# Kernel optimization log

Measured on AMD Instinct MI355X. Metric: run time of the kernel, lower is better.

## Reference

```python
import jax, jax.numpy as jnp
import numpy as np
import math

N_HEAD = 16

def setup_inputs() -> dict:
    key = jax.random.key(0)
    ks = jax.random.split(key, 8)
    B, S, P, NX = 4, 1024, 128, 1024
    return {
        "x": jax.random.normal(ks[0], (B, S, NX), jnp.float32),
        "M": jax.random.normal(ks[1], (B, P, NX), jnp.float32),
        "Mmask": jnp.ones((B, P), jnp.float32),
        "attention_mask": jnp.zeros((B, 1, 1, S), jnp.float32),
        "W_attn": jax.random.normal(ks[2], (NX, 3 * NX), jnp.float32) * 0.02,
        "b_attn": jnp.zeros((3 * NX,), jnp.float32),
        "W_mem": jax.random.normal(ks[3], (NX, 2 * NX), jnp.float32) * 0.02,
        "b_mem": jnp.zeros((2 * NX,), jnp.float32),
        "W_proj": jax.random.normal(ks[4], (NX, NX), jnp.float32) * 0.02,
        "b_proj": jnp.zeros((NX,), jnp.float32),
    }

def _split_heads(t, H):
    B, T, NX = t.shape
    return t.reshape(B, T, H, NX // H).transpose(0, 2, 1, 3)  # [B,H,T,dh]

def reference(x, M, Mmask, attention_mask, W_attn, b_attn, W_mem, b_mem, W_proj, b_proj):
    B, S, NX = x.shape
    H = N_HEAD
    dh = NX // H
    P = M.shape[1]

    # fused QKV projection (Conv1D == x @ W + b)
    qkv = x @ W_attn + b_attn
    q, k, v = jnp.split(qkv, 3, axis=2)

    # memory K/V projection, prepended along the key/value sequence axis
    ekv = M @ W_mem + b_mem
    ek, ev = jnp.split(ekv, 2, axis=2)
    key = jnp.concatenate([ek, k], axis=1)   # [B, P+S, NX]
    value = jnp.concatenate([ev, v], axis=1)

    qh = _split_heads(q, H)      # [B,H,S,dh]
    kh = _split_heads(key, H)    # [B,H,P+S,dh]
    vh = _split_heads(value, H)  # [B,H,P+S,dh]

    w = jnp.einsum('bhsd,bhtd->bhst', qh, kh) / math.sqrt(dh)  # [B,H,S,P+S]

    # causal bias over the self part, all-ones over the memory part
    causal = jnp.tril(jnp.ones((S, S), w.dtype))
    b = jnp.concatenate([jnp.ones((S, P), w.dtype), causal], axis=1)[None, None]  # [1,1,S,P+S]
    w = w * b - 10000.0 * (1.0 - b)

    # additive attention mask: memory-mask bias concatenated before token mask
    mem_bias = (1.0 - Mmask)[:, None, None, :] * -10000.0  # [B,1,1,P]
    am = jnp.concatenate([mem_bias, jnp.broadcast_to(attention_mask, (B, 1, 1, S))], axis=3)
    w = w + am

    w = jax.nn.softmax(w, axis=-1)
    a = jnp.einsum('bhst,bhtd->bhsd', w, vh)                  # [B,H,S,dh]
    a = a.transpose(0, 2, 1, 3).reshape(B, S, NX)             # merge heads
    return a @ W_proj + b_proj
```

## Files before the change

kernel.cpp:

```cpp
#include <hip/hip_runtime.h>
#include <hip/hip_bf16.h>


typedef __attribute__((ext_vector_type(8))) short bf16x8;
typedef __attribute__((ext_vector_type(4))) float f32x4;

#define MFMA16(a, b, c) __builtin_amdgcn_mfma_f32_16x16x32_bf16((a), (b), (c), 0, 0, 0)

#define GLOAD_LDS16(g, l)                                                  \
    __builtin_amdgcn_global_load_lds(                                      \
        (const __attribute__((address_space(1))) void*)(const void*)(g),   \
        (__attribute__((address_space(3))) void*)(void*)(l), 16, 0, 0)

static __device__ __forceinline__ unsigned short f2bf(float f) {
    union { float f; unsigned int u; } v; v.f = f;
    unsigned int u = v.u;
    return (unsigned short)((u + 0x7fffu + ((u >> 16) & 1u)) >> 16);
}

__global__ void cvt_all(const float* __restrict__ x, const float* __restrict__ Mem,
                        unsigned short* __restrict__ x_bf, unsigned short* __restrict__ M_bf) {
    int i = blockIdx.x * 256 + threadIdx.x;
    if (i < 1048576) {
        float4 v = ((const float4*)x)[i];
        ushort4 o; o.x = f2bf(v.x); o.y = f2bf(v.y); o.z = f2bf(v.z); o.w = f2bf(v.w);
        ((ushort4*)x_bf)[i] = o;
    } else {
        int j = i - 1048576;
        float4 v = ((const float4*)Mem)[j];
        ushort4 o; o.x = f2bf(v.x); o.y = f2bf(v.y); o.z = f2bf(v.z); o.w = f2bf(v.w);
        ((ushort4*)M_bf)[j] = o;
    }
}

static __device__ __forceinline__ void transpose_body(const float* __restrict__ W,
                                                      unsigned short* __restrict__ Wt,
                                                      int K, int N, int bx, int by,
                                                      float (*tile)[33]) {
    int n0 = bx * 32, k0 = by * 32;
    int tx = threadIdx.x & 31, ty = threadIdx.x >> 5;
    #pragma unroll
    for (int r = ty; r < 32; r += 8) tile[r][tx] = W[(size_t)(k0 + r) * N + n0 + tx];
    __syncthreads();
    #pragma unroll
    for (int r = ty; r < 32; r += 8) Wt[(size_t)(n0 + r) * K + k0 + tx] = f2bf(tile[tx][r]);
}

__global__ void prep_weights(const float* __restrict__ W_attn, const float* __restrict__ W_mem,
                             const float* __restrict__ W_proj, unsigned short* __restrict__ Wat,
                             unsigned short* __restrict__ Wmt, unsigned short* __restrict__ Wpt,
                             const float* __restrict__ Mmask, const float* __restrict__ amask,
                             float* __restrict__ biasT) {
    __shared__ float tile[32][33];
    int bid = blockIdx.x;
    if (bid < 3072) {
        transpose_body(W_attn, Wat, 1024, 3072, bid % 96, bid / 96, tile);
    } else if (bid < 5120) {
        int t = bid - 3072; transpose_body(W_mem, Wmt, 1024, 2048, t % 64, t / 64, tile);
    } else if (bid < 6144) {
        int t = bid - 5120; transpose_body(W_proj, Wpt, 1024, 1024, t % 32, t / 32, tile);
    } else {
        int i = (bid - 6144) * 256 + threadIdx.x;
        if (i < 4 * 1152) {
            int b = i / 1152, t = i % 1152;
            float v = (t < 128) ? (Mmask[b * 128 + t] - 1.f) * 10000.f
                                : amask[b * 1024 + t - 128];
            biasT[i] = v * 1.4426950408889634f;
        }
    }
}

__global__ __launch_bounds__(256) void build_kv(const unsigned short* __restrict__ QKV,
                                                const unsigned short* __restrict__ EKV,
                                                unsigned short* __restrict__ Kc,
                                                unsigned short* __restrict__ Vt) {
    __shared__ unsigned short vt[64][72];
    const int tid = threadIdx.x;
    const int blk = blockIdx.x;
    const int tc = blk % 18, bh = blk / 18;
    const int h = bh & 15, b = bh >> 4;
    const int row = tid >> 2, c = (tid & 3) * 16;
    const int tg = tc * 64 + row;
    const unsigned short* src;
    if (tg < 128) src = EKV + (size_t)(b * 128 + tg) * 2048 + h * 64 + c;
    else          src = QKV + (size_t)(b * 1024 + tg - 128) * 3072 + 1024 + h * 64 + c;
    bf16x8 ka = *(const bf16x8*)src;
    bf16x8 kb = *(const bf16x8*)(src + 8);
    bf16x8 va = *(const bf16x8*)(src + 1024);
    bf16x8 vb = *(const bf16x8*)(src + 1032);
    unsigned short* kd = Kc + (size_t)bh * 73728 + (size_t)tg * 64 + c;
    *(bf16x8*)kd = ka;
    *(bf16x8*)(kd + 8) = kb;
    *(bf16x8*)&vt[row][c] = va;
    *(bf16x8*)&vt[row][c + 8] = vb;
    __syncthreads();
    bf16x8 o0, o1;
    #pragma unroll
    for (int j = 0; j < 8; j++) { o0[j] = vt[c + j][row]; o1[j] = vt[c + 8 + j][row]; }
    unsigned short* vd = Vt + (size_t)bh * 73728 + (size_t)row * 1152 + tc * 64 + c;
    *(bf16x8*)vd = o0;
    *(bf16x8*)(vd + 8) = o1;
}

template <int TN, int STORE_BF16>
static __device__ __forceinline__ void gemm_body(const unsigned short* __restrict__ A,
                                                 const unsigned short* __restrict__ Bt,
                                                 const float* __restrict__ bias,
                                                 void* __restrict__ C, int bm, int bn,
                                                 int N, int K,
                                                 unsigned short* As, unsigned short* Bs) {
    constexpr int NJ = TN / 32;
    constexpr int NCH = 8 + TN / 16;
    const int tid = threadIdx.x;
    const int lane = tid & 63, wave = tid >> 6;
    const int quad = lane >> 4, l16 = lane & 15;
    const int wm = (wave & 1) * 64, wn = (wave >> 1) * (TN / 2);
    const int crow = lane >> 2, ccol = (lane & 3) * 8;
    const unsigned short* Abase = A + (size_t)(bm * 128 + crow) * K + ccol;
    const unsigned short* Bbase = Bt + (size_t)(bn * TN + crow) * K + ccol;

    f32x4 acc[4][NJ] = {};
    for (int k0 = 0; k0 < K; k0 += 32) {
        __syncthreads();
        #pragma unroll
        for (int cc = 0; cc < NCH / 4; cc++) {
            const int c = wave * (NCH / 4) + cc;
            if (c < 8) GLOAD_LDS16(Abase + (size_t)(c * 16) * K + k0, &As[c * 512]);
            else       GLOAD_LDS16(Bbase + (size_t)((c - 8) * 16) * K + k0, &Bs[(c - 8) * 512]);
        }
        __syncthreads();
        bf16x8 af[4], bf[NJ];
        #pragma unroll
        for (int i = 0; i < 4; i++) af[i] = *(const bf16x8*)&As[(wm + i * 16 + l16) * 32 + quad * 8];
        #pragma unroll
        for (int j = 0; j < NJ; j++) bf[j] = *(const bf16x8*)&Bs[(wn + j * 16 + l16) * 32 + quad * 8];
        #pragma unroll
        for (int i = 0; i < 4; i++)
            #pragma unroll
            for (int j = 0; j < NJ; j++)
                acc[i][j] = MFMA16(af[i], bf[j], acc[i][j]);
    }
    float bj[NJ];
    #pragma unroll
    for (int j = 0; j < NJ; j++) bj[j] = bias[bn * TN + wn + j * 16 + l16];
    #pragma unroll
    for (int i = 0; i < 4; i++) {
        const int row = bm * 128 + wm + i * 16 + quad * 4;
        #pragma unroll
        for (int j = 0; j < NJ; j++) {
            const int col = bn * TN + wn + j * 16 + l16;
            #pragma unroll
            for (int r = 0; r < 4; r++) {
                float v = acc[i][j][r] + bj[j];
                if (STORE_BF16)
                    ((unsigned short*)C)[(size_t)(row + r) * N + col] = f2bf(v);
                else
                    ((float*)C)[(size_t)(row + r) * N + col] = v;
            }
        }
    }
}

__global__ __launch_bounds__(256) void gemm_qkv_ekv(const unsigned short* __restrict__ x_bf,
                                                    const unsigned short* __restrict__ Wat,
                                                    const float* __restrict__ b_attn,
                                                    unsigned short* __restrict__ QKV,
                                                    const unsigned short* __restrict__ M_bf,
                                                    const unsigned short* __restrict__ Wmt,
                                                    const float* __restrict__ b_mem,
                                                    unsigned short* __restrict__ EKV) {
    __shared__ unsigned short As[128 * 32];
    __shared__ unsigned short Bs[128 * 32];
    const int bid = blockIdx.x;
    if (bid < 768)
        gemm_body<128, 1>(x_bf, Wat, b_attn, QKV, bid & 31, bid >> 5, 3072, 1024, As, Bs);
    else {
        const int t = bid - 768;
        gemm_body<128, 1>(M_bf, Wmt, b_mem, EKV, t & 3, t >> 2, 2048, 1024, As, Bs);
    }
}

__global__ __launch_bounds__(256) void gemm_proj(const unsigned short* __restrict__ Abuf,
                                                 const unsigned short* __restrict__ Wpt,
                                                 const float* __restrict__ b_proj,
                                                 float* __restrict__ out) {
    __shared__ unsigned short As[128 * 32];
    __shared__ unsigned short Bs[64 * 32];
    const int bid = blockIdx.x;
    gemm_body<64, 0>(Abuf, Wpt, b_proj, out, bid & 31, bid >> 5, 1024, 1024, As, Bs);
}

__global__ __launch_bounds__(256) void attn_kernel(const unsigned short* __restrict__ QKV,
                                                   const unsigned short* __restrict__ Kc,
                                                   const unsigned short* __restrict__ Vt,
                                                   const float* __restrict__ biasT,
                                                   unsigned short* __restrict__ Aout) {
    __shared__ char smem[34304];
    float* On = (float*)smem;
    float* Dn = (float*)(smem + 33792);
    unsigned short* Ps = (unsigned short*)smem;
    const int tid = threadIdx.x;
    const int lane = tid & 63, wave = tid >> 6;
    const int quad = lane >> 4, l16 = lane & 15;
    const int blk = blockIdx.x;
    const int qg = 31 - (blk >> 6);
    const int bh = blk & 63;
    const int h = bh & 15, b = bh >> 4;
    const int qrow0 = qg * 32;

    bf16x8 qf[2][2];
    #pragma unroll
    for (int sm = 0; sm < 2; sm++)
        #pragma unroll
        for (int k2 = 0; k2 < 2; k2++)
            qf[sm][k2] = *(const bf16x8*)(QKV + (size_t)(b * 1024 + qrow0 + sm * 16 + l16) * 3072 +
                                          h * 64 + k2 * 32 + quad * 8);

    const unsigned short* Kb = Kc + (size_t)bh * 73728;
    const unsigned short* Vb = Vt + (size_t)bh * 73728;
    const float* bias_b = biasT + b * 1152;

    bf16x8 ones;
    #pragma unroll
    for (int j = 0; j < 8; j++) ones[j] = (short)0x3F80;

    f32x4 o[2][4] = {};
    f32x4 oden[2] = {};
    const int tmax = min(1152, ((qrow0 + 223) >> 6) << 6);

    for (int t0 = wave * 64; t0 < tmax; t0 += 256) {
        bf16x8 kf[4][2], vf[2][4];
        #pragma unroll
        for (int tn = 0; tn < 4; tn++) {
            const unsigned short* kp = Kb + (size_t)(t0 + tn * 16 + l16) * 64 + quad * 8;
            kf[tn][0] = *(const bf16x8*)kp;
            kf[tn][1] = *(const bf16x8*)(kp + 32);
        }
        #pragma unroll
        for (int tk = 0; tk < 2; tk++)
            #pragma unroll
            for (int dn = 0; dn < 4; dn++)
                vf[tk][dn] = *(const bf16x8*)(Vb + (size_t)(dn * 16 + l16) * 1152 +
                                              t0 + tk * 32 + quad * 8);
        float4 bt[4];
        #pragma unroll
        for (int tn = 0; tn < 4; tn++)
            bt[tn] = *(const float4*)(bias_b + t0 + tn * 16 + quad * 4);

        const bool nomask = (t0 + 63 <= 128 + qrow0);
        #pragma unroll
        for (int sm = 0; sm < 2; sm++) {
            const int sg = qrow0 + sm * 16 + l16;
            #pragma unroll
            for (int tn = 0; tn < 4; tn++) {
                f32x4 st = {};
                st = MFMA16(kf[tn][0], qf[sm][0], st);
                st = MFMA16(kf[tn][1], qf[sm][1], st);
                float p[4];
                #pragma unroll
                for (int r = 0; r < 4; r++) {
                    float e = __builtin_amdgcn_exp2f(st[r] * 0.18033688011112042f + bt[tn][r]);
                    if (!nomask) {
                        const int tg = t0 + tn * 16 + quad * 4 + r;
                        e = (tg < 128 || tg - 128 <= sg) ? e : 0.f;
                    }
                    p[r] = e;
                }
                union { ushort4 u; __hip_bfloat162 h2[2]; } pk;
                pk.h2[0] = __float22bfloat162_rn(float2{p[0], p[1]});
                pk.h2[1] = __float22bfloat162_rn(float2{p[2], p[3]});
                *(ushort4*)&Ps[wave * 2304 + (sm * 16 + l16) * 72 + tn * 16 + quad * 4] = pk.u;
            }
        }
        #pragma unroll
        for (int sm = 0; sm < 2; sm++) {
            #pragma unroll
            for (int tk = 0; tk < 2; tk++) {
                bf16x8 pf = *(const bf16x8*)&Ps[wave * 2304 + (sm * 16 + l16) * 72 +
                                                tk * 32 + quad * 8];
                oden[sm] = MFMA16(pf, ones, oden[sm]);
                #pragma unroll
                for (int dn = 0; dn < 4; dn++)
                    o[sm][dn] = MFMA16(pf, vf[tk][dn], o[sm][dn]);
            }
        }
    }

    __syncthreads();
    #pragma unroll
    for (int sm = 0; sm < 2; sm++) {
        #pragma unroll
        for (int dn = 0; dn < 4; dn++)
            #pragma unroll
            for (int r = 0; r < 4; r++)
                On[wave * 2112 + (sm * 16 + quad * 4 + r) * 66 + dn * 16 + l16] = o[sm][dn][r];
        if (l16 == 0)
            #pragma unroll
            for (int r = 0; r < 4; r++)
                Dn[wave * 32 + sm * 16 + quad * 4 + r] = oden[sm][r];
    }
    __syncthreads();

    const int row = tid >> 3, c0 = (tid & 7) * 8;
    float den = 0.f, a8[8] = {};
    #pragma unroll
    for (int w = 0; w < 4; w++) {
        den += Dn[w * 32 + row];
        #pragma unroll
        for (int j = 0; j < 8; j++) a8[j] += On[w * 2112 + row * 66 + c0 + j];
    }
    const float inv = 1.f / den;
    bf16x8 o8;
    #pragma unroll
    for (int j = 0; j < 8; j++) o8[j] = (short)f2bf(a8[j] * inv);
    *(bf16x8*)&Aout[(size_t)(b * 1024 + qrow0 + row) * 1024 + h * 64 + c0] = o8;
}

extern "C" void kernel_launch(void* const* d_in, const int* in_sizes, int n_in,
                              void* d_out, int out_size, void* d_ws, size_t ws_size,
                              hipStream_t stream) {
    const float* x      = (const float*)d_in[0];
    const float* Mem    = (const float*)d_in[1];
    const float* Mmask  = (const float*)d_in[2];
    const float* amask  = (const float*)d_in[3];
    const float* W_attn = (const float*)d_in[4];
    const float* b_attn = (const float*)d_in[5];
    const float* W_mem  = (const float*)d_in[6];
    const float* b_mem  = (const float*)d_in[7];
    const float* W_proj = (const float*)d_in[8];
    const float* b_proj = (const float*)d_in[9];
    float* out = (float*)d_out;

    char* ws = (char*)d_ws;
    unsigned short* x_bf  = (unsigned short*)ws;  ws += (size_t)4096 * 1024 * 2;
    unsigned short* M_bf  = (unsigned short*)ws;  ws += (size_t)512 * 1024 * 2;
    unsigned short* Wat   = (unsigned short*)ws;  ws += (size_t)3072 * 1024 * 2;
    unsigned short* Wmt   = (unsigned short*)ws;  ws += (size_t)2048 * 1024 * 2;
    unsigned short* Wpt   = (unsigned short*)ws;  ws += (size_t)1024 * 1024 * 2;
    unsigned short* QKV   = (unsigned short*)ws;  ws += (size_t)4096 * 3072 * 2;
    unsigned short* EKV   = (unsigned short*)ws;  ws += (size_t)512 * 2048 * 2;
    unsigned short* Abuf  = (unsigned short*)ws;  ws += (size_t)4096 * 1024 * 2;
    unsigned short* Kc    = (unsigned short*)ws;  ws += (size_t)64 * 1152 * 64 * 2;
    unsigned short* Vt    = (unsigned short*)ws;  ws += (size_t)64 * 64 * 1152 * 2;
    float*          biasT = (float*)ws;           ws += (size_t)4 * 1152 * 4;

    cvt_all<<<4608, 256, 0, stream>>>(x, Mem, x_bf, M_bf);
    prep_weights<<<6163, 256, 0, stream>>>(W_attn, W_mem, W_proj, Wat, Wmt, Wpt,
                                           Mmask, amask, biasT);
    gemm_qkv_ekv<<<832, 256, 0, stream>>>(x_bf, Wat, b_attn, QKV, M_bf, Wmt, b_mem, EKV);
    build_kv<<<1152, 256, 0, stream>>>(QKV, EKV, Kc, Vt);
    attn_kernel<<<2048, 256, 0, stream>>>(QKV, Kc, Vt, biasT, Abuf);
    gemm_proj<<<512, 256, 0, stream>>>(Abuf, Wpt, b_proj, out);
}
```

Measured before the change: 237.4 us.

## Restructure attention to share LDS-staged K/V tiles across waves per query block

The attention kernel now gives each block 64 query rows, one 16-row slice per wave. All four waves stream the same 64-key K/V tile, staged once into LDS with global_load_lds. Previously each wave loaded its own key range and the partial results were reduced across waves through shared memory. The change removes that cross-wave reduction and the redundant per-wave global K/V loads, and remaps block indices so the heads of one XCD stay together for L2 locality. In exchange it adds two barriers per key tile, halves the grid, and writes the output with scalar bf16 stores.

```diff
diff --git a/kernel.cpp b/kernel.cpp
--- a/kernel.cpp
+++ b/kernel.cpp
@@ -195,67 +195,71 @@
                                                    const unsigned short* __restrict__ Vt,
                                                    const float* __restrict__ biasT,
                                                    unsigned short* __restrict__ Aout) {
-    __shared__ char smem[34304];
-    float* On = (float*)smem;
-    float* Dn = (float*)(smem + 33792);
-    unsigned short* Ps = (unsigned short*)smem;
+    __shared__ unsigned short Ks[2 * 64 * 32];
+    __shared__ unsigned short Vs[2 * 64 * 32];
+    __shared__ unsigned short Ps[4][16 * 72];
     const int tid = threadIdx.x;
     const int lane = tid & 63, wave = tid >> 6;
     const int quad = lane >> 4, l16 = lane & 15;
     const int blk = blockIdx.x;
-    const int qg = 31 - (blk >> 6);
-    const int bh = blk & 63;
+    const int xcd = blk & 7, idx = blk >> 3;
+    const int bh = xcd * 8 + (idx >> 4);
+    const int qg = 15 - (idx & 15);
     const int h = bh & 15, b = bh >> 4;
-    const int qrow0 = qg * 32;
-
-    bf16x8 qf[2][2];
-    #pragma unroll
-    for (int sm = 0; sm < 2; sm++)
-        #pragma unroll
-        for (int k2 = 0; k2 < 2; k2++)
-            qf[sm][k2] = *(const bf16x8*)(QKV + (size_t)(b * 1024 + qrow0 + sm * 16 + l16) * 3072 +
-                                          h * 64 + k2 * 32 + quad * 8);
+    const int qrow0 = qg * 64;
+    const int qrow_w = qrow0 + wave * 16;
+
+    bf16x8 qf[2];
+    #pragma unroll
+    for (int k2 = 0; k2 < 2; k2++)
+        qf[k2] = *(const bf16x8*)(QKV + (size_t)(b * 1024 + qrow_w + l16) * 3072 +
+                                  h * 64 + k2 * 32 + quad * 8);
 
     const unsigned short* Kb = Kc + (size_t)bh * 73728;
     const unsigned short* Vb = Vt + (size_t)bh * 73728;
     const float* bias_b = biasT + b * 1152;
 
+    const int srow = lane >> 2;
+    const int sc8 = (lane & 3) * 8;
+
     bf16x8 ones;
     #pragma unroll
     for (int j = 0; j < 8; j++) ones[j] = (short)0x3F80;
 
-    f32x4 o[2][4] = {};
-    f32x4 oden[2] = {};
-    const int tmax = min(1152, ((qrow0 + 223) >> 6) << 6);
-
-    for (int t0 = wave * 64; t0 < tmax; t0 += 256) {
-        bf16x8 kf[4][2], vf[2][4];
-        #pragma unroll
-        for (int tn = 0; tn < 4; tn++) {
-            const unsigned short* kp = Kb + (size_t)(t0 + tn * 16 + l16) * 64 + quad * 8;
-            kf[tn][0] = *(const bf16x8*)kp;
-            kf[tn][1] = *(const bf16x8*)(kp + 32);
-        }
-        #pragma unroll
-        for (int tk = 0; tk < 2; tk++)
-            #pragma unroll
-            for (int dn = 0; dn < 4; dn++)
-                vf[tk][dn] = *(const bf16x8*)(Vb + (size_t)(dn * 16 + l16) * 1152 +
-                                              t0 + tk * 32 + quad * 8);
-        float4 bt[4];
-        #pragma unroll
-        for (int tn = 0; tn < 4; tn++)
-            bt[tn] = *(const float4*)(bias_b + t0 + tn * 16 + quad * 4);
-
-        const bool nomask = (t0 + 63 <= 128 + qrow0);
-        #pragma unroll
-        for (int sm = 0; sm < 2; sm++) {
-            const int sg = qrow0 + sm * 16 + l16;
+    f32x4 o[4] = {};
+    f32x4 oden = {};
+    const int tmax = min(1152, qrow0 + 192);
+
+    for (int t0 = 0; t0 < tmax; t0 += 64) {
+        __syncthreads();
+        #pragma unroll
+        for (int cc = 0; cc < 4; cc++) {
+            const int c = wave * 4 + cc;
+            if (c < 8) {
+                const int kk = c & 1, rch = c >> 1;
+                GLOAD_LDS16(Kb + (size_t)(t0 + rch * 16 + srow) * 64 + kk * 32 + sc8,
+                            &Ks[kk * 2048 + rch * 512]);
+            } else {
+                const int c2 = c - 8, tk = c2 & 1, dch = c2 >> 1;
+                GLOAD_LDS16(Vb + (size_t)(dch * 16 + srow) * 1152 + t0 + tk * 32 + sc8,
+                            &Vs[tk * 2048 + dch * 512]);
+            }
+        }
+        __syncthreads();
+        if (t0 <= qrow_w + 143) {
+            const bool nomask = (t0 + 63 <= 128 + qrow_w);
+            float4 bt[4];
+            #pragma unroll
+            for (int tn = 0; tn < 4; tn++)
+                bt[tn] = *(const float4*)(bias_b + t0 + tn * 16 + quad * 4);
+            const int sg = qrow_w + l16;
             #pragma unroll
             for (int tn = 0; tn < 4; tn++) {
+                bf16x8 kf0 = *(const bf16x8*)&Ks[0 * 2048 + (tn * 16 + l16) * 32 + quad * 8];
+                bf16x8 kf1 = *(const bf16x8*)&Ks[1 * 2048 + (tn * 16 + l16) * 32 + quad * 8];
                 f32x4 st = {};
-                st = MFMA16(kf[tn][0], qf[sm][0], st);
-                st = MFMA16(kf[tn][1], qf[sm][1], st);
+                st = MFMA16(kf0, qf[0], st);
+                st = MFMA16(kf1, qf[1], st);
                 float p[4];
                 #pragma unroll
                 for (int r = 0; r < 4; r++) {
@@ -269,51 +273,29 @@
                 union { ushort4 u; __hip_bfloat162 h2[2]; } pk;
                 pk.h2[0] = __float22bfloat162_rn(float2{p[0], p[1]});
                 pk.h2[1] = __float22bfloat162_rn(float2{p[2], p[3]});
-                *(ushort4*)&Ps[wave * 2304 + (sm * 16 + l16) * 72 + tn * 16 + quad * 4] = pk.u;
+                *(ushort4*)&Ps[wave][l16 * 72 + tn * 16 + quad * 4] = pk.u;
             }
-        }
-        #pragma unroll
-        for (int sm = 0; sm < 2; sm++) {
             #pragma unroll
             for (int tk = 0; tk < 2; tk++) {
-                bf16x8 pf = *(const bf16x8*)&Ps[wave * 2304 + (sm * 16 + l16) * 72 +
-                                                tk * 32 + quad * 8];
-                oden[sm] = MFMA16(pf, ones, oden[sm]);
+                bf16x8 pf = *(const bf16x8*)&Ps[wave][l16 * 72 + tk * 32 + quad * 8];
+                oden = MFMA16(pf, ones, oden);
                 #pragma unroll
-                for (int dn = 0; dn < 4; dn++)
-                    o[sm][dn] = MFMA16(pf, vf[tk][dn], o[sm][dn]);
+                for (int dn = 0; dn < 4; dn++) {
+                    bf16x8 vf = *(const bf16x8*)&Vs[tk * 2048 + (dn * 16 + l16) * 32 + quad * 8];
+                    o[dn] = MFMA16(pf, vf, o[dn]);
+                }
             }
         }
     }
 
-    __syncthreads();
-    #pragma unroll
-    for (int sm = 0; sm < 2; sm++) {
+    #pragma unroll
+    for (int r = 0; r < 4; r++) {
+        const float inv = 1.f / oden[r];
+        const size_t orow = (size_t)(b * 1024 + qrow_w + quad * 4 + r) * 1024 + h * 64;
         #pragma unroll
         for (int dn = 0; dn < 4; dn++)
-            #pragma unroll
-            for (int r = 0; r < 4; r++)
-                On[wave * 2112 + (sm * 16 + quad * 4 + r) * 66 + dn * 16 + l16] = o[sm][dn][r];
-        if (l16 == 0)
-            #pragma unroll
-            for (int r = 0; r < 4; r++)
-                Dn[wave * 32 + sm * 16 + quad * 4 + r] = oden[sm][r];
-    }
-    __syncthreads();
-
-    const int row = tid >> 3, c0 = (tid & 7) * 8;
-    float den = 0.f, a8[8] = {};
-    #pragma unroll
-    for (int w = 0; w < 4; w++) {
-        den += Dn[w * 32 + row];
-        #pragma unroll
-        for (int j = 0; j < 8; j++) a8[j] += On[w * 2112 + row * 66 + c0 + j];
-    }
-    const float inv = 1.f / den;
-    bf16x8 o8;
-    #pragma unroll
-    for (int j = 0; j < 8; j++) o8[j] = (short)f2bf(a8[j] * inv);
-    *(bf16x8*)&Aout[(size_t)(b * 1024 + qrow0 + row) * 1024 + h * 64 + c0] = o8;
+            Aout[orow + dn * 16 + l16] = f2bf(o[dn][r] * inv);
+    }
 }
 
 extern "C" void kernel_launch(void* const* d_in, const int* in_sizes, int n_in,
@@ -349,6 +331,6 @@
                                            Mmask, amask, biasT);
     gemm_qkv_ekv<<<832, 256, 0, stream>>>(x_bf, Wat, b_attn, QKV, M_bf, Wmt, b_mem, EKV);
     build_kv<<<1152, 256, 0, stream>>>(QKV, EKV, Kc, Vt);
-    attn_kernel<<<2048, 256, 0, stream>>>(QKV, Kc, Vt, biasT, Abuf);
+    attn_kernel<<<1024, 256, 0, stream>>>(QKV, Kc, Vt, biasT, Abuf);
     gemm_proj<<<512, 256, 0, stream>>>(Abuf, Wpt, b_proj, out);
 }
```

New measurement: 227.5 us. -4.2%, faster.
